# Kernel tuning notes

Hardware: AMD Instinct MI355X
Metric: run time of the kernel (lower is better)

## Reference

```python
import jax, jax.numpy as jnp
import numpy as np

B, S, H, NUM_ITEM = 4096, 50, 64, 40000


def setup_inputs() -> dict:
    key = jax.random.key(0)
    ks = jax.random.split(key, 6)
    return {
        "all_memory": jax.random.normal(ks[0], (B, S, H), dtype=jnp.float32),
        "last_memory": jax.random.normal(ks[1], (B, H), dtype=jnp.float32),
        "Wr": jax.random.normal(ks[2], (H, H), dtype=jnp.float32) * 0.1,
        "Ur": jax.random.normal(ks[3], (H, H), dtype=jnp.float32) * 0.1,
        "Vr_w": jax.random.normal(ks[4], (1, H), dtype=jnp.float32) * 0.1,
        "Vr_b": jnp.zeros((1,), dtype=jnp.float32),
        "seq_item": jax.random.randint(ks[5], (B, S), 0, NUM_ITEM),
    }


def reference(all_memory, last_memory, Wr, Ur, Vr_w, Vr_b, seq_item):
    # Additive attention scores (dropout is identity at inference / p=0).
    am = jnp.einsum('bsh,ih->bsi', all_memory, Ur)        # [B,S,H]
    lm = jnp.einsum('bh,ih->bi', last_memory, Wr)[:, None, :]  # [B,1,H]
    scores = jnp.einsum('bsh,oh->bso', jnp.tanh(lm + am), Vr_w)[..., 0] + Vr_b[0]  # [B,S]
    probs = jax.nn.softmax(scores, axis=-1)               # [B,S]
    # Scatter attention mass onto the item vocabulary. This is mathematically
    # identical to the original one-hot build_map + matmul (duplicate items in
    # a sequence accumulate, just as in the dense GEMM).
    b_idx = jnp.arange(probs.shape[0])[:, None]           # [B,1]
    out = jnp.zeros((probs.shape[0], NUM_ITEM), dtype=probs.dtype)
    out = out.at[b_idx, seq_item].add(probs)              # [B,NUM_ITEM]
    return out
```

## Files before the change

### kernel.cpp

```cpp
#include <hip/hip_runtime.h>
#include <math.h>

#define NB 4096
#define NS 50
#define NH 64
#define NITEM 40000

typedef float f4 __attribute__((ext_vector_type(4)));

__global__ __launch_bounds__(256) void fused_zero_probs(
    const float* __restrict__ all_memory,
    const float* __restrict__ last_memory,
    const float* __restrict__ Wr,
    const float* __restrict__ Ur,
    const float* __restrict__ Vr_w,
    const float* __restrict__ Vr_b,
    float* __restrict__ out,
    float* __restrict__ probs,
    int compute_blocks)
{
    const int bid = blockIdx.x;
    if (bid >= compute_blocks) {
        const long long total4 = (long long)NB * NITEM / 4;
        f4* o4 = (f4*)out;
        long long idx = (long long)(bid - compute_blocks) * blockDim.x + threadIdx.x;
        const long long stride = (long long)(gridDim.x - compute_blocks) * blockDim.x;
        f4 z = (f4)(0.0f);
        for (long long i = idx; i < total4; i += stride)
            __builtin_nontemporal_store(z, o4 + i);
        return;
    }

    const int lane = threadIdx.x & 63;
    const int warp = __builtin_amdgcn_readfirstlane((int)(threadIdx.x >> 6));
    const int b = bid * 4 + warp;

    float ur[NH];
    {
        const float* urow = Ur + lane * NH;
        #pragma unroll
        for (int h = 0; h < NH; h += 4) {
            float4 u = *(const float4*)(urow + h);
            ur[h] = u.x; ur[h + 1] = u.y; ur[h + 2] = u.z; ur[h + 3] = u.w;
        }
    }

    float lm = 0.f;
    {
        const float* lrow = last_memory + b * NH;
        const float* wrow = Wr + lane * NH;
        #pragma unroll
        for (int h = 0; h < NH; h += 4) {
            float4 w = *(const float4*)(wrow + h);
            float4 l = *(const float4*)(lrow + h);
            lm += w.x * l.x + w.y * l.y + w.z * l.z + w.w * l.w;
        }
    }

    const float vw = Vr_w[lane];
    const float vb = Vr_b[0];
    const float* am = all_memory + (long long)b * (NS * NH);

    float myscore = 0.f;
    for (int s = 0; s < NS; ++s) {
        const float* arow = am + s * NH;
        float v0 = 0.f, v1 = 0.f, v2 = 0.f, v3 = 0.f;
        #pragma unroll
        for (int h = 0; h < NH; h += 4) {
            float4 a = *(const float4*)(arow + h);
            v0 += a.x * ur[h];
            v1 += a.y * ur[h + 1];
            v2 += a.z * ur[h + 2];
            v3 += a.w * ur[h + 3];
        }
        float t = tanhf(lm + ((v0 + v1) + (v2 + v3))) * vw;
        #pragma unroll
        for (int off = 32; off >= 1; off >>= 1)
            t += __shfl_xor(t, off, 64);
        t += vb;
        myscore = (lane == s) ? t : myscore;
    }

    float sc = (lane < NS) ? myscore : -INFINITY;
    float m = sc;
    #pragma unroll
    for (int off = 32; off >= 1; off >>= 1)
        m = fmaxf(m, __shfl_xor(m, off, 64));
    float e = (lane < NS) ? expf(sc - m) : 0.f;
    float d = e;
    #pragma unroll
    for (int off = 32; off >= 1; off >>= 1)
        d += __shfl_xor(d, off, 64);
    if (lane < NS)
        probs[b * NS + lane] = e / d;
}

__global__ __launch_bounds__(256) void scatter_k(
    const float* __restrict__ probs,
    const int* __restrict__ seq,
    float* __restrict__ out)
{
    int t = blockIdx.x * 256 + threadIdx.x;
    if (t >= NB * NS) return;
    int b = t / NS;
    float p = probs[t];
    int item = seq[t];
    atomicAdd(out + (long long)b * NITEM + item, p);
}

extern "C" void kernel_launch(void* const* d_in, const int* in_sizes, int n_in,
                              void* d_out, int out_size, void* d_ws, size_t ws_size,
                              hipStream_t stream) {
    const float* all_memory  = (const float*)d_in[0];
    const float* last_memory = (const float*)d_in[1];
    const float* Wr          = (const float*)d_in[2];
    const float* Ur          = (const float*)d_in[3];
    const float* Vr_w        = (const float*)d_in[4];
    const float* Vr_b        = (const float*)d_in[5];
    const int*   seq         = (const int*)d_in[6];
    float* out   = (float*)d_out;
    float* probs = (float*)d_ws;

    const int compute_blocks = NB / 4;
    const int zero_blocks    = 1024;
    fused_zero_probs<<<compute_blocks + zero_blocks, 256, 0, stream>>>(
        all_memory, last_memory, Wr, Ur, Vr_w, Vr_b, out, probs, compute_blocks);

    scatter_k<<<(NB * NS + 255) / 256, 256, 0, stream>>>(probs, seq, out);
}
```

Baseline: 181.0 us.

## Fuse score, zero-fill and scatter into one block-per-row kernel

Replaces the two-kernel scheme (compute plus separate zero blocks, then a scatter kernel) with one kernel where each block owns a batch row. The block computes its 50 scores split across 4 warps, zeroes its own output row, runs the softmax in one warp, and atomically adds the probabilities into the row it just zeroed. This removes the second launch and the probs round trip through global memory. It drops the nontemporal stores and the Vr_b add, which is safe only because softmax is shift-invariant. Each block also reloads Ur and Wr per row.

```diff
diff --git a/kernel.cpp b/kernel.cpp
--- a/kernel.cpp
+++ b/kernel.cpp
@@ -5,35 +5,26 @@
 #define NS 50
 #define NH 64
 #define NITEM 40000
+#define ROW4 (NITEM / 4)
 
 typedef float f4 __attribute__((ext_vector_type(4)));
 
-__global__ __launch_bounds__(256) void fused_zero_probs(
+__global__ __launch_bounds__(256) void fused_row(
     const float* __restrict__ all_memory,
     const float* __restrict__ last_memory,
     const float* __restrict__ Wr,
     const float* __restrict__ Ur,
     const float* __restrict__ Vr_w,
-    const float* __restrict__ Vr_b,
-    float* __restrict__ out,
-    float* __restrict__ probs,
-    int compute_blocks)
+    const int* __restrict__ seq,
+    float* __restrict__ out)
 {
-    const int bid = blockIdx.x;
-    if (bid >= compute_blocks) {
-        const long long total4 = (long long)NB * NITEM / 4;
-        f4* o4 = (f4*)out;
-        long long idx = (long long)(bid - compute_blocks) * blockDim.x + threadIdx.x;
-        const long long stride = (long long)(gridDim.x - compute_blocks) * blockDim.x;
-        f4 z = (f4)(0.0f);
-        for (long long i = idx; i < total4; i += stride)
-            __builtin_nontemporal_store(z, o4 + i);
-        return;
-    }
+    __shared__ float sLDS[NS];
+    __shared__ float pLDS[NS];
 
-    const int lane = threadIdx.x & 63;
-    const int warp = __builtin_amdgcn_readfirstlane((int)(threadIdx.x >> 6));
-    const int b = bid * 4 + warp;
+    const int b = blockIdx.x;
+    const int tid = (int)threadIdx.x;
+    const int lane = tid & 63;
+    const int warp = __builtin_amdgcn_readfirstlane(tid >> 6);
 
     float ur[NH];
     {
@@ -44,7 +35,6 @@
             ur[h] = u.x; ur[h + 1] = u.y; ur[h + 2] = u.z; ur[h + 3] = u.w;
         }
     }
-
     float lm = 0.f;
     {
         const float* lrow = last_memory + b * NH;
@@ -56,13 +46,10 @@
             lm += w.x * l.x + w.y * l.y + w.z * l.z + w.w * l.w;
         }
     }
-
     const float vw = Vr_w[lane];
-    const float vb = Vr_b[0];
     const float* am = all_memory + (long long)b * (NS * NH);
 
-    float myscore = 0.f;
-    for (int s = 0; s < NS; ++s) {
+    for (int s = warp; s < NS; s += 4) {
         const float* arow = am + s * NH;
         float v0 = 0.f, v1 = 0.f, v2 = 0.f, v3 = 0.f;
         #pragma unroll
@@ -77,35 +64,35 @@
         #pragma unroll
         for (int off = 32; off >= 1; off >>= 1)
             t += __shfl_xor(t, off, 64);
-        t += vb;
-        myscore = (lane == s) ? t : myscore;
+        if (lane == 0) sLDS[s] = t;
     }
 
-    float sc = (lane < NS) ? myscore : -INFINITY;
-    float m = sc;
-    #pragma unroll
-    for (int off = 32; off >= 1; off >>= 1)
-        m = fmaxf(m, __shfl_xor(m, off, 64));
-    float e = (lane < NS) ? expf(sc - m) : 0.f;
-    float d = e;
-    #pragma unroll
-    for (int off = 32; off >= 1; off >>= 1)
-        d += __shfl_xor(d, off, 64);
-    if (lane < NS)
-        probs[b * NS + lane] = e / d;
-}
+    f4* orow4 = (f4*)(out + (long long)b * NITEM);
+    const f4 z = (f4)(0.0f);
+    for (int i = tid; i < ROW4; i += 256)
+        orow4[i] = z;
 
-__global__ __launch_bounds__(256) void scatter_k(
-    const float* __restrict__ probs,
-    const int* __restrict__ seq,
-    float* __restrict__ out)
-{
-    int t = blockIdx.x * 256 + threadIdx.x;
-    if (t >= NB * NS) return;
-    int b = t / NS;
-    float p = probs[t];
-    int item = seq[t];
-    atomicAdd(out + (long long)b * NITEM + item, p);
+    __syncthreads();
+
+    if (warp == 0) {
+        float sc = (lane < NS) ? sLDS[lane] : -INFINITY;
+        float m = sc;
+        #pragma unroll
+        for (int off = 32; off >= 1; off >>= 1)
+            m = fmaxf(m, __shfl_xor(m, off, 64));
+        float e = (lane < NS) ? expf(sc - m) : 0.f;
+        float d = e;
+        #pragma unroll
+        for (int off = 32; off >= 1; off >>= 1)
+            d += __shfl_xor(d, off, 64);
+        if (lane < NS) pLDS[lane] = e / d;
+    }
+    __syncthreads();
+
+    if (tid < NS) {
+        int item = seq[b * NS + tid];
+        atomicAdd(out + (long long)b * NITEM + item, pLDS[tid]);
+    }
 }
 
 extern "C" void kernel_launch(void* const* d_in, const int* in_sizes, int n_in,
@@ -116,15 +103,9 @@
     const float* Wr          = (const float*)d_in[2];
     const float* Ur          = (const float*)d_in[3];
     const float* Vr_w        = (const float*)d_in[4];
-    const float* Vr_b        = (const float*)d_in[5];
     const int*   seq         = (const int*)d_in[6];
-    float* out   = (float*)d_out;
-    float* probs = (float*)d_ws;
+    float* out = (float*)d_out;
 
-    const int compute_blocks = NB / 4;
-    const int zero_blocks    = 1024;
-    fused_zero_probs<<<compute_blocks + zero_blocks, 256, 0, stream>>>(
-        all_memory, last_memory, Wr, Ur, Vr_w, Vr_b, out, probs, compute_blocks);
-
-    scatter_k<<<(NB * NS + 255) / 256, 256, 0, stream>>>(probs, seq, out);
+    fused_row<<<NB, 256, 0, stream>>>(all_memory, last_memory, Wr, Ur, Vr_w,
+                                      seq, out);
 }
```

Result: slower. 279.5 us (+54.4%).
